# Kernel optimization log

Measured on AMD Instinct MI355X. Metric: run time of the kernel, lower is better.

Reference implementation:

```python
import jax, jax.numpy as jnp
import numpy as np

N = 65536      # total nodes (cells) in batch
E = 262144     # edges per edge type
T = 3          # edge types: row, col, diag
D = 128        # hidden_dim
HG = 4         # gat_heads
DHG = D // HG  # 32, GAT head dim
HH = 4         # hgt_heads
DHH = D // HH  # 32, HGT head dim
B = 32         # boards per batch
SLOPE = 0.2
EPS = 1e-6


def setup_inputs():
    ks = jax.random.split(jax.random.key(0), 32)
    def nrm(i, shape, s=0.05):
        return (jax.random.normal(ks[i], shape) * s).astype(jnp.float32)
    inp = {
        'x_cell': nrm(0, (N, D), 1.0),
        'z_h': nrm(1, (B, D), 1.0),
        'x_cell_embedded': nrm(2, (N, D), 1.0),
        'edge_index': jax.random.randint(ks[3], (T, 2, E), 0, N, dtype=jnp.int32),
        'batch_size': B,
        # GAT conv 1 (one GATConv per edge type, summed)
        'gat1_W': nrm(4, (T, D, D), 0.09),
        'gat1_asrc': nrm(5, (T, HG, DHG), 0.12),
        'gat1_adst': nrm(6, (T, HG, DHG), 0.12),
        'gat1_b': jnp.zeros((T, D), jnp.float32),
        # GAT conv 2
        'gat2_W': nrm(7, (T, D, D), 0.09),
        'gat2_asrc': nrm(8, (T, HG, DHG), 0.12),
        'gat2_adst': nrm(9, (T, HG, DHG), 0.12),
        'gat2_b': jnp.zeros((T, D), jnp.float32),
        # RMSNorms
        'norm1_s': jnp.ones((D,), jnp.float32),
        'norm2_s': jnp.ones((D,), jnp.float32),
        'norm3_s': jnp.ones((D,), jnp.float32),
        # HGT (single node type 'cell', T edge types)
        'hgt_Wk': nrm(10, (D, D), 0.09), 'hgt_bk': jnp.zeros((D,), jnp.float32),
        'hgt_Wq': nrm(11, (D, D), 0.09), 'hgt_bq': jnp.zeros((D,), jnp.float32),
        'hgt_Wv': nrm(12, (D, D), 0.09), 'hgt_bv': jnp.zeros((D,), jnp.float32),
        'hgt_arel': nrm(13, (T, HH, DHH, DHH), 0.15),
        'hgt_mrel': nrm(14, (T, HH, DHH, DHH), 0.15),
        'hgt_prel': jnp.ones((T, HH), jnp.float32),
        'hgt_Wo': nrm(15, (D, D), 0.09), 'hgt_bo': jnp.zeros((D,), jnp.float32),
        'hgt_skip': jnp.ones((), jnp.float32),
        # input injection
        'inj_W': nrm(16, (D, D), 0.09), 'inj_b': jnp.zeros((D,), jnp.float32),
        # FiLM
        'film_W1': nrm(17, (D, 2 * D), 0.09), 'film_b1': jnp.zeros((2 * D,), jnp.float32),
        'film_W2': nrm(18, (2 * D, 2 * D), 0.001), 'film_b2': jnp.zeros((2 * D,), jnp.float32),
    }
    return inp


def _rmsnorm(x, scale):
    return scale * x * jax.lax.rsqrt(jnp.mean(x * x, axis=-1, keepdims=True) + EPS)


def _res(x_old, x_new, scale):
    return jax.nn.leaky_relu(x_old + _rmsnorm(x_new, scale), SLOPE)


def _gat_sum(x, W, asrc, adst, b, src, dst):
    """HeteroConv(sum) over T GATConvs (concat heads, add_self_loops)."""
    loop = jnp.arange(N, dtype=src.dtype)
    def one(Wt, a_s, a_d, bt, s, t):
        s = jnp.concatenate([s, loop])   # self loops
        t = jnp.concatenate([t, loop])
        h = (x @ Wt).reshape(N, HG, DHG)             # [N,H,Dh]
        alpha_src = (h * a_s).sum(-1)                # [N,H]
        alpha_dst = (h * a_d).sum(-1)
        e = jax.nn.leaky_relu(alpha_src[s] + alpha_dst[t], SLOPE)  # [E+N,H]
        m = jax.ops.segment_max(e, t, num_segments=N)
        ex = jnp.exp(e - m[t])
        denom = jax.ops.segment_sum(ex, t, num_segments=N)
        alpha = ex / (denom[t] + 1e-16)
        out = jax.ops.segment_sum(alpha[:, :, None] * h[s], t, num_segments=N)
        return out.reshape(N, D) + bt
    return jax.vmap(one)(W, asrc, adst, b, src, dst).sum(0)


def _hgt(x, Wk, bk, Wq, bq, Wv, bv, a_rel, m_rel, p_rel, Wo, bo, skip, src, dst):
    k = (x @ Wk + bk).reshape(N, HH, DHH)
    q = (x @ Wq + bq).reshape(N, HH, DHH)
    v = (x @ Wv + bv).reshape(N, HH, DHH)
    # per-edge-type relation transforms at node level, then gather per edge
    k_t = jnp.einsum('nhd,thdf->tnhf', k, a_rel)    # [T,N,H,Dk]
    v_t = jnp.einsum('nhd,thdf->tnhf', v, m_rel)
    k_e = jax.vmap(lambda a, i: a[i])(k_t, src)     # [T,E,H,Dk]
    v_e = jax.vmap(lambda a, i: a[i])(v_t, src)
    score = (q[dst] * k_e).sum(-1) * p_rel[:, None, :] / np.sqrt(DHH)  # [T,E,H]
    score = score.reshape(T * E, HH)
    dst_f = dst.reshape(-1)
    m = jax.ops.segment_max(score, dst_f, num_segments=N)
    ex = jnp.exp(score - m[dst_f])
    denom = jax.ops.segment_sum(ex, dst_f, num_segments=N)
    alpha = ex / (denom[dst_f] + 1e-16)
    agg = jax.ops.segment_sum(alpha[:, :, None] * v_e.reshape(T * E, HH, DHH),
                              dst_f, num_segments=N)          # [N,H,Dk]
    out = jax.nn.gelu(agg.reshape(N, D), approximate=False) @ Wo + bo
    sig = jax.nn.sigmoid(skip)
    return sig * out + (1.0 - sig) * x


def _film(nodes, z_h, W1, b1, W2, b2, bsz):
    gb = jax.nn.gelu(z_h @ W1 + b1, approximate=False) @ W2 + b2  # [B,2D]
    gamma, beta = jnp.split(gb, 2, axis=-1)
    gamma = 0.1 * jnp.tanh(gamma)
    beta = 0.1 * jnp.tanh(beta)
    c = N // bsz
    out = (1.0 + gamma)[:, None, :] * nodes.reshape(bsz, c, D) + beta[:, None, :]
    return out.reshape(N, D)


def reference(x_cell, z_h, x_cell_embedded,
              gat1_W, gat1_asrc, gat1_adst, gat1_b,
              gat2_W, gat2_asrc, gat2_adst, gat2_b,
              norm1_s, norm2_s, norm3_s,
              hgt_Wk, hgt_bk, hgt_Wq, hgt_bq, hgt_Wv, hgt_bv,
              hgt_arel, hgt_mrel, hgt_prel, hgt_Wo, hgt_bo, hgt_skip,
              inj_W, inj_b, film_W1, film_b1, film_W2, film_b2,
              edge_index, batch_size):
    src = edge_index[:, 0]
    dst = edge_index[:, 1]
    x1 = _res(x_cell, _gat_sum(x_cell, gat1_W, gat1_asrc, gat1_adst, gat1_b, src, dst), norm1_s)
    x2 = _res(x1, _gat_sum(x1, gat2_W, gat2_asrc, gat2_adst, gat2_b, src, dst), norm2_s)
    x3 = _res(x2, _hgt(x2, hgt_Wk, hgt_bk, hgt_Wq, hgt_bq, hgt_Wv, hgt_bv,
                       hgt_arel, hgt_mrel, hgt_prel, hgt_Wo, hgt_bo, hgt_skip,
                       src, dst), norm3_s)
    x3 = x3 + x_cell_embedded @ inj_W + inj_b
    return _film(x3, z_h, film_W1, film_b1, film_W2, film_b2, batch_size)
```

## Files before the change

kernel.cpp:

```cpp
#include <hip/hip_runtime.h>

#define NN 65536
#define EE 262144
#define ND ((size_t)NN * 128)
#define TBW 132
#define WLP 136
#define NTOT (EE + NN)
#define CSRN (3*EE + 3*NN)

typedef unsigned short u16;
typedef unsigned char u8;
typedef short bf8_t __attribute__((ext_vector_type(8)));
typedef float f32x4 __attribute__((ext_vector_type(4)));
typedef float f32x2 __attribute__((ext_vector_type(2)));

__device__ __forceinline__ float lrelu(float x){ return x > 0.f ? x : 0.2f*x; }
__device__ __forceinline__ float gelu_exact(float x){ return 0.5f*x*(1.f+erff(x*0.70710678118654752f)); }
__device__ __forceinline__ float fexp(float x){ return __expf(x); }
__device__ __forceinline__ u16 f2bf(float f){
    union { float f; unsigned u; } v; v.f = f;
    unsigned u = v.u;
    return (u16)((u + 0x7FFFu + ((u >> 16) & 1u)) >> 16);
}
__device__ __forceinline__ float bf2f(u16 b){
    union { unsigned u; float f; } v; v.u = ((unsigned)b) << 16; return v.f;
}
__device__ __forceinline__ float2 bf2x(unsigned p){
    union { unsigned u; float f; } a, b;
    a.u = (p & 0xFFFFu) << 16; b.u = p & 0xFFFF0000u;
    return make_float2(a.f, b.f);
}
__device__ __forceinline__ unsigned cvt2(float a, float b){
    unsigned r; asm("v_cvt_pk_bf16_f32 %0, %1, %2" : "=v"(r) : "v"(a), "v"(b)); return r;
}
__device__ __forceinline__ unsigned enc_fp8x4(float a, float b, float c, float d){
    int r = __builtin_amdgcn_cvt_pk_fp8_f32(a, b, 0, false);
    r = __builtin_amdgcn_cvt_pk_fp8_f32(c, d, r, true);
    return (unsigned)r;
}

__device__ __forceinline__ void load_af32(const float* __restrict__ X, int row, int lk, bf8_t* af){
    #pragma unroll
    for (int kk = 0; kk < 4; ++kk){
        const float* p = X + (size_t)row*128 + kk*32 + lk*8;
        float4 a = *(const float4*)p;
        float4 b = *(const float4*)(p+4);
        union { bf8_t v; unsigned u[4]; } r;
        r.u[0] = cvt2(a.x, a.y); r.u[1] = cvt2(a.z, a.w);
        r.u[2] = cvt2(b.x, b.y); r.u[3] = cvt2(b.z, b.w);
        af[kk] = r.v;
    }
}
__device__ __forceinline__ void load_af16(const u16* __restrict__ X, int row, int lk, bf8_t* af){
    #pragma unroll
    for (int kk = 0; kk < 4; ++kk)
        af[kk] = *(const bf8_t*)(X + (size_t)row*128 + kk*32 + lk*8);
}

__device__ __forceinline__ void stage_w(const u16* __restrict__ src, u16* __restrict__ wl, int tid){
    #pragma unroll
    for (int j = 0; j < 8; ++j){
        int o = (j*256 + tid)*8;
        bf8_t v = *(const bf8_t*)(src + o);
        *(bf8_t*)(wl + ((o>>7)*WLP + (o&127))) = v;
    }
}

__device__ __forceinline__ void mfma_l1_acc(const bf8_t* af, const u16* __restrict__ wl,
                                            int lr, int lk, f32x4* acc){
    #pragma unroll
    for (int kk = 0; kk < 4; ++kk){
        bf8_t B[8];
        #pragma unroll
        for (int nt = 0; nt < 8; ++nt)
            B[nt] = *(const bf8_t*)&wl[(nt*16+lr)*WLP + kk*32 + lk*8];
        #pragma unroll
        for (int nt = 0; nt < 8; ++nt)
            acc[nt] = __builtin_amdgcn_mfma_f32_16x16x32_bf16(af[kk], B[nt], acc[nt], 0, 0, 0);
    }
}
__device__ __forceinline__ void mfma_l1(const bf8_t* af, const u16* __restrict__ wl,
                                        int lr, int lk, f32x4* acc){
    #pragma unroll
    for (int i = 0; i < 8; ++i) acc[i] = (f32x4){0.f,0.f,0.f,0.f};
    mfma_l1_acc(af, wl, lr, lk, acc);
}
__device__ __forceinline__ void mfma_l2(const bf8_t* af0, const bf8_t* af1,
                                        const u16* __restrict__ wl,
                                        int lr, int lk, f32x4* acc0, f32x4* acc1){
    #pragma unroll
    for (int i = 0; i < 8; ++i){ acc0[i] = (f32x4){0.f,0.f,0.f,0.f}; acc1[i] = (f32x4){0.f,0.f,0.f,0.f}; }
    #pragma unroll
    for (int kk = 0; kk < 4; ++kk){
        bf8_t B[8];
        #pragma unroll
        for (int nt = 0; nt < 8; ++nt)
            B[nt] = *(const bf8_t*)&wl[(nt*16+lr)*WLP + kk*32 + lk*8];
        #pragma unroll
        for (int nt = 0; nt < 8; ++nt){
            acc0[nt] = __builtin_amdgcn_mfma_f32_16x16x32_bf16(af0[kk], B[nt], acc0[nt], 0, 0, 0);
            acc1[nt] = __builtin_amdgcn_mfma_f32_16x16x32_bf16(af1[kk], B[nt], acc1[nt], 0, 0, 0);
        }
    }
}
__device__ __forceinline__ void mfma_bd1_acc(const bf8_t* af, const u16* __restrict__ Bp,
                                             int lr, int lk, f32x4* acc){
    bf8_t B[8];
    #pragma unroll
    for (int nt = 0; nt < 8; ++nt)
        B[nt] = *(const bf8_t*)&Bp[nt*512 + lr*32 + lk*8];
    #pragma unroll
    for (int nt = 0; nt < 8; ++nt)
        acc[nt] = __builtin_amdgcn_mfma_f32_16x16x32_bf16(af[nt>>1], B[nt], acc[nt], 0, 0, 0);
}
__device__ __forceinline__ void mfma_bd2(const bf8_t* af0, const bf8_t* af1,
                                         const u16* __restrict__ Bp,
                                         int lr, int lk, f32x4* acc0, f32x4* acc1){
    bf8_t B[8];
    #pragma unroll
    for (int nt = 0; nt < 8; ++nt)
        B[nt] = *(const bf8_t*)&Bp[nt*512 + lr*32 + lk*8];
    #pragma unroll
    for (int nt = 0; nt < 8; ++nt){
        acc0[nt] = __builtin_amdgcn_mfma_f32_16x16x32_bf16(af0[nt>>1], B[nt], (f32x4){0.f,0.f,0.f,0.f}, 0, 0, 0);
        acc1[nt] = __builtin_amdgcn_mfma_f32_16x16x32_bf16(af1[nt>>1], B[nt], (f32x4){0.f,0.f,0.f,0.f}, 0, 0, 0);
    }
}

__device__ __forceinline__ void acc_to_tb(u16 (*tbw)[TBW], const f32x4* acc, int lr, int lk, const float* bias){
    asm volatile("s_waitcnt lgkmcnt(0)" ::: "memory");
    #pragma unroll
    for (int nt = 0; nt < 8; ++nt){
        int col = nt*16 + lr;
        float badd = bias ? bias[col] : 0.f;
        #pragma unroll
        for (int i = 0; i < 4; ++i) tbw[lk*4+i][col] = f2bf(acc[nt][i] + badd);
    }
    asm volatile("s_waitcnt lgkmcnt(0)" ::: "memory");
}
__device__ __forceinline__ void acc_to_tb_gelu(u16 (*tbw)[TBW], const f32x4* acc, int lr, int lk){
    asm volatile("s_waitcnt lgkmcnt(0)" ::: "memory");
    #pragma unroll
    for (int nt = 0; nt < 8; ++nt){
        int col = nt*16 + lr;
        #pragma unroll
        for (int i = 0; i < 4; ++i) tbw[lk*4+i][col] = f2bf(gelu_exact(acc[nt][i]));
    }
    asm volatile("s_waitcnt lgkmcnt(0)" ::: "memory");
}
__device__ __forceinline__ void tb_store(const u16 (*tbw)[TBW], u16* __restrict__ O, size_t rowstride, int rowbase, int lr, int lk){
    #pragma unroll
    for (int c = 0; c < 4; ++c){
        bf8_t v = *(const bf8_t*)&tbw[c*4+lk][lr*8];
        *(bf8_t*)(O + (size_t)(rowbase + c*4 + lk)*rowstride + lr*8) = v;
    }
}
__device__ __forceinline__ void tb_store_fp8(const u16 (*tbw)[TBW], u8* __restrict__ O, size_t rowstride, int rowbase, int lr, int lk){
    #pragma unroll
    for (int c = 0; c < 4; ++c){
        bf8_t v = *(const bf8_t*)&tbw[c*4+lk][lr*8];
        float f[8];
        #pragma unroll
        for (int j = 0; j < 8; ++j) f[j] = bf2f((u16)v[j]);
        uint2 o2;
        o2.x = enc_fp8x4(f[0], f[1], f[2], f[3]);
        o2.y = enc_fp8x4(f[4], f[5], f[6], f[7]);
        *(uint2*)(O + (size_t)(rowbase + c*4 + lk)*rowstride + lr*8) = o2;
    }
}
__device__ __forceinline__ void tb_frags(const u16 (*tbw)[TBW], int lr, int lk, bf8_t* ha){
    #pragma unroll
    for (int kk = 0; kk < 4; ++kk) ha[kk] = *(const bf8_t*)&tbw[lr][kk*32 + lk*8];
}
__device__ __forceinline__ void tb_rows(const u16 (*tbw)[TBW], int lr, int lk, bf8_t* rw){
    #pragma unroll
    for (int c = 0; c < 4; ++c) rw[c] = *(const bf8_t*)&tbw[c*4+lk][lr*8];
}

__global__ __launch_bounds__(256) void xcast_k(const float* __restrict__ X, u16* __restrict__ O){
    size_t gid = (size_t)blockIdx.x*256 + threadIdx.x;
    const float* p = X + gid*8;
    float4 a = *(const float4*)p;
    float4 b = *(const float4*)(p+4);
    union { bf8_t v; unsigned u[4]; } r;
    r.u[0] = cvt2(a.x, a.y); r.u[1] = cvt2(a.z, a.w);
    r.u[2] = cvt2(b.x, b.y); r.u[3] = cvt2(b.z, b.w);
    *(bf8_t*)(O + gid*8) = r.v;
}

__global__ __launch_bounds__(256) void wpack_k(
    const float* __restrict__ g1W, const float* __restrict__ g2W,
    const float* __restrict__ Wk, const float* __restrict__ Wq, const float* __restrict__ Wv,
    const float* __restrict__ Wo, const float* __restrict__ injW,
    const float* __restrict__ arel, const float* __restrict__ mrel,
    const float* __restrict__ g1as, const float* __restrict__ g1ad,
    const float* __restrict__ g2as, const float* __restrict__ g2ad,
    u16* __restrict__ wp, u16* __restrict__ wpa)
{
    int b = blockIdx.x, tid = threadIdx.x;
    if (b < 11) {
        const float* src;
        if (b < 3) src = g1W + b*16384;
        else if (b < 6) src = g2W + (b-3)*16384;
        else if (b == 6) src = Wk;
        else if (b == 7) src = Wq;
        else if (b == 8) src = Wv;
        else if (b == 9) src = Wo;
        else src = injW;
        u16* dst = wp + (size_t)b*16384;
        for (int idx = tid; idx < 16384; idx += 256) {
            int n = idx >> 7, k = idx & 127;
            dst[idx] = f2bf(src[k*128 + n]);
        }
    } else if (b < 17) {
        int rel2 = (b < 14);
        const float* src = rel2 ? (arel + (b-11)*4096) : (mrel + (b-14)*4096);
        u16* dst = wp + (size_t)11*16384 + (size_t)(b-11)*4096;
        for (int idx = tid; idx < 4096; idx += 256) {
            int nt = idx >> 9, rest = idx & 511;
            int lr = rest >> 5, kp = rest & 31;
            int h = nt >> 1, c = (nt & 1)*16 + lr;
            float v = rel2 ? src[h*1024 + c*32 + kp] : src[h*1024 + kp*32 + c];
            dst[idx] = f2bf(v);
        }
    } else {
        for (int idx = tid; idx < 6*2048; idx += 256) {
            int m = idx >> 11;
            int j = idx & 2047;
            int cg = j >> 7, k = j & 127;
            const float* as = (m < 3) ? g1as : g2as;
            const float* ad = (m < 3) ? g1ad : g2ad;
            int t = (m < 3) ? m : m - 3;
            float v = 0.f;
            if (cg < 4)      { if ((k>>5)==cg)   v = as[t*128 + cg*32 + (k&31)]; }
            else if (cg < 8) { int g = cg-4; if ((k>>5)==g) v = ad[t*128 + g*32 + (k&31)]; }
            wpa[idx] = f2bf(v);
        }
    }
}

__global__ __launch_bounds__(256, 3) void gat_gemm3_k(const u16* __restrict__ Xb,
    const u16* __restrict__ wpg, const u16* __restrict__ wpa,
    u16* __restrict__ hb, float* __restrict__ alsb, float* __restrict__ aldb)
{
    __shared__ __align__(16) u16 wl[128*WLP];
    __shared__ __align__(16) u16 tb[4][16][TBW];
    const int tid = threadIdx.x, wave = tid>>6, lane = tid&63, lr = lane&15, lk = lane>>4;
    const int t = blockIdx.y;
    const int rw0 = blockIdx.x*128 + wave*32;
    bf8_t af0[4], af1[4];
    load_af16(Xb, rw0 + lr, lk, af0);
    load_af16(Xb, rw0 + 16 + lr, lk, af1);
    stage_w(wpg + t*16384, wl, tid);
    bf8_t Ba[4];
    #pragma unroll
    for (int kk = 0; kk < 4; ++kk)
        Ba[kk] = *(const bf8_t*)&wpa[t*2048 + lr*128 + kk*32 + lk*8];
    __syncthreads();
    f32x4 acc0[8], acc1[8];
    mfma_l2(af0, af1, wl, lr, lk, acc0, acc1);
    u16* h = hb + (size_t)t*ND;
    float* alst = alsb + (size_t)t*NN*4;
    float* aldt = aldb + (size_t)t*NN*4;
    {
        acc_to_tb(tb[wave], acc0, lr, lk, nullptr);
        tb_store(tb[wave], h, 128, rw0, lr, lk);
        bf8_t ha[4]; tb_frags(tb[wave], lr, lk, ha);
        f32x4 a2 = (f32x4){0.f,0.f,0.f,0.f};
        #pragma unroll
        for (int kk = 0; kk < 4; ++kk)
            a2 = __builtin_amdgcn_mfma_f32_16x16x32_bf16(ha[kk], Ba[kk], a2, 0, 0, 0);
        if (lr < 8){
            float* dp = (lr < 4) ? alst : aldt;
            int g = lr & 3;
            #pragma unroll
            for (int i = 0; i < 4; ++i) dp[(size_t)(rw0 + lk*4 + i)*4 + g] = a2[i];
        }
    }
    {
        acc_to_tb(tb[wave], acc1, lr, lk, nullptr);
        tb_store(tb[wave], h, 128, rw0 + 16, lr, lk);
        bf8_t ha[4]; tb_frags(tb[wave], lr, lk, ha);
        f32x4 a2 = (f32x4){0.f,0.f,0.f,0.f};
        #pragma unroll
        for (int kk = 0; kk < 4; ++kk)
            a2 = __builtin_amdgcn_mfma_f32_16x16x32_bf16(ha[kk], Ba[kk], a2, 0, 0, 0);
        if (lr < 8){
            float* dp = (lr < 4) ? alst : aldt;
            int g = lr & 3;
            #pragma unroll
            for (int i = 0; i < 4; ++i) dp[(size_t)(rw0 + 16 + lk*4 + i)*4 + g] = a2[i];
        }
    }
}

__global__ __launch_bounds__(256, 3) void hgt_proj_k(const u16* __restrict__ X,
    const u16* __restrict__ wpk, const u16* __restrict__ wpq, const u16* __restrict__ wpv,
    const u16* __restrict__ wpad,
    const float* __restrict__ bk, const float* __restrict__ bq, const float* __restrict__ bv,
    u8* __restrict__ kvb, u16* __restrict__ qtb)
{
    __shared__ __align__(16) u16 wl[128*WLP];
    __shared__ __align__(16) u16 tb[4][16][TBW];
    const int tid = threadIdx.x, wave = tid>>6, lane = tid&63, lr = lane&15, lk = lane>>4;
    const int task = blockIdx.y;
    const int rw0 = blockIdx.x*128 + wave*32;
    bf8_t af0[4], af1[4];
    load_af16(X, rw0 + lr, lk, af0);
    load_af16(X, rw0 + 16 + lr, lk, af1);
    f32x4 acc0[8], acc1[8];
    if (task == 0) {
        stage_w(wpk, wl, tid);
        __syncthreads();
        mfma_l2(af0, af1, wl, lr, lk, acc0, acc1);
        acc_to_tb(tb[wave], acc0, lr, lk, bk); tb_store_fp8(tb[wave], kvb, 256, rw0, lr, lk);
        acc_to_tb(tb[wave], acc1, lr, lk, bk); tb_store_fp8(tb[wave], kvb, 256, rw0 + 16, lr, lk);
    } else if (task == 1) {
        stage_w(wpv, wl, tid);
        __syncthreads();
        mfma_l2(af0, af1, wl, lr, lk, acc0, acc1);
        acc_to_tb(tb[wave], acc0, lr, lk, bv); tb_store_fp8(tb[wave], kvb + 128, 256, rw0, lr, lk);
        acc_to_tb(tb[wave], acc1, lr, lk, bv); tb_store_fp8(tb[wave], kvb + 128, 256, rw0 + 16, lr, lk);
    } else {
        const int t = task - 2;
        stage_w(wpq, wl, tid);
        __syncthreads();
        mfma_l2(af0, af1, wl, lr, lk, acc0, acc1);
        bf8_t ha0[4], ha1[4];
        acc_to_tb(tb[wave], acc0, lr, lk, bq); tb_frags(tb[wave], lr, lk, ha0);
        acc_to_tb(tb[wave], acc1, lr, lk, bq); tb_frags(tb[wave], lr, lk, ha1);
        mfma_bd2(ha0, ha1, wpad + t*4096, lr, lk, acc0, acc1);
        u16* o = qtb + (size_t)t*ND;
        acc_to_tb(tb[wave], acc0, lr, lk, nullptr); tb_store(tb[wave], o, 128, rw0, lr, lk);
        acc_to_tb(tb[wave], acc1, lr, lk, nullptr); tb_store(tb[wave], o, 128, rw0 + 16, lr, lk);
    }
}

__global__ __launch_bounds__(256) void hist_k(const int* __restrict__ ei, int* __restrict__ cnt){
    int gid = blockIdx.x*256 + threadIdx.x;
    int t = gid / EE, e = gid - t*EE;
    int d = ei[t*2*EE + EE + e];
    atomicAdd(&cnt[t*NN + d], 1);
}
__global__ __launch_bounds__(256) void scanA_k(const int* __restrict__ cnt, int* __restrict__ s0off, int* __restrict__ parts){
    __shared__ int sums[256];
    int b = blockIdx.x; int base = b * 1024;
    int tid = threadIdx.x;
    int v[4]; int tsum = 0;
    #pragma unroll
    for (int i = 0; i < 4; ++i){
        int n = base + tid*4 + i;
        v[i] = cnt[n] + cnt[NN+n] + cnt[2*NN+n] + 3;
        tsum += v[i];
    }
    sums[tid] = tsum; __syncthreads();
    for (int ofs = 1; ofs < 256; ofs <<= 1) {
        int a = (tid >= ofs) ? sums[tid-ofs] : 0;
        __syncthreads();
        sums[tid] += a;
        __syncthreads();
    }
    int run = sums[tid] - tsum;
    #pragma unroll
    for (int i = 0; i < 4; ++i){ s0off[base + tid*4 + i] = run; run += v[i]; }
    if (tid == 255) parts[b] = sums[255];
}
__global__ void scan2_k(int* parts){
    if (threadIdx.x == 0 && blockIdx.x == 0) {
        int run = 0;
        for (int i = 0; i < 64; ++i) { int v = parts[i]; parts[i] = run; run += v; }
    }
}
__global__ __launch_bounds__(256) void scanB_k(const int* __restrict__ cnt, int* __restrict__ s0off,
                                               int* __restrict__ s1off, int* __restrict__ s2off,
                                               const int* __restrict__ parts){
    int b = blockIdx.x; int base = b * 1024;
    int add = parts[b];
    #pragma unroll
    for (int i = 0; i < 4; ++i){
        int n = base + threadIdx.x*4 + i;
        int m = s0off[n] + add;
        int c0 = cnt[n], c1 = cnt[NN+n];
        s0off[n] = m;
        s1off[n] = m + c0 + 1;
        s2off[n] = m + c0 + c1 + 2;
    }
    if (b == 0 && threadIdx.x == 0) s0off[NN] = CSRN;
}
__global__ __launch_bounds__(256) void selffill_k(const int* __restrict__ s0off, const int* __restrict__ s1off,
                                                  const int* __restrict__ s2off, int* __restrict__ csrc){
    int gid = blockIdx.x*256 + threadIdx.x;
    int t = gid / NN, n = gid - t*NN;
    int pos = (t==0) ? s0off[n] : (t==1 ? s1off[n] : s2off[n]);
    csrc[pos] = n;
}
__global__ __launch_bounds__(256) void scatter_k(const int* __restrict__ ei,
    const int* __restrict__ s0off, const int* __restrict__ s1off, const int* __restrict__ s2off,
    int* __restrict__ cur, int* __restrict__ csrc, int* __restrict__ posmap){
    int gid = blockIdx.x*256 + threadIdx.x;
    int t = gid / EE, e = gid - t*EE;
    int s = ei[t*2*EE + e];
    int d = ei[t*2*EE + EE + e];
    int p = atomicAdd(&cur[t*NN + d], 1);
    int basep = (t==0) ? s0off[d] : (t==1 ? s1off[d] : s2off[d]);
    int pos = basep + 1 + p;
    csrc[pos] = s;
    posmap[t*EE + e] = pos;
}

__global__ __launch_bounds__(256) void alpha_k(const float* __restrict__ alsb, const float* __restrict__ aldb,
    const int* __restrict__ ei, const int* __restrict__ posmap,
    const int* __restrict__ s0off, const int* __restrict__ s1off, const int* __restrict__ s2off,
    float4* __restrict__ ab)
{
    int gid = blockIdx.x*256 + threadIdx.x;
    int t = gid / NTOT, r = gid - t*NTOT;
    int s, d, pos;
    if (r < EE) {
        s = ei[t*2*EE + r];
        d = ei[t*2*EE + EE + r];
        pos = posmap[t*EE + r];
    } else {
        int n = r - EE;
        s = n; d = n;
        pos = (t==0) ? s0off[n] : (t==1 ? s1off[n] : s2off[n]);
    }
    const float* As = alsb + ((size_t)t*NN + s)*4;
    const float* Ad = aldb + ((size_t)t*NN + d)*4;
    float4 o;
    o.x = fexp(lrelu(As[0] + Ad[0]));
    o.y = fexp(lrelu(As[1] + Ad[1]));
    o.z = fexp(lrelu(As[2] + Ad[2]));
    o.w = fexp(lrelu(As[3] + Ad[3]));
    ab[pos] = o;
}

__global__ __launch_bounds__(256) void gat_aggres_k(const u16* __restrict__ hb,
    const float* __restrict__ abf,
    const int* __restrict__ s0off, const int* __restrict__ s1off, const int* __restrict__ s2off,
    const int* __restrict__ csrc,
    const float* __restrict__ bias3, const u16* __restrict__ xoldb,
    const float* __restrict__ scale, u16* __restrict__ outb)
{
    int gid = blockIdx.x*256 + threadIdx.x;
    int node = gid >> 6, lane = gid & 63;
    int eh = lane >> 5, hh = (lane >> 3) & 3, cp = lane & 7;
    int ch = hh*32 + cp*4;
    int segb[4] = { s0off[node], s1off[node], s2off[node], s0off[node+1] };
    float a[4] = {0.f, 0.f, 0.f, 0.f};
    #pragma unroll
    for (int t = 0; t < 3; ++t) {
        const u16* h = hb + (size_t)t*ND;
        int beg = segb[t], end = segb[t+1];
        float ds = 0.f, s0 = 0.f, s1 = 0.f, s2 = 0.f, s3 = 0.f;
        for (int pos = beg; pos < end; pos += 4) {
            int p0 = pos + eh, p1 = pos + 2 + eh;
            int v0 = (p0 < end), v1 = (p1 < end);
            int q0 = v0 ? p0 : beg, q1 = v1 ? p1 : beg;
            int sA = csrc[q0], sB = csrc[q1];
            float alA = abf[(size_t)q0*4 + hh];
            float alB = abf[(size_t)q1*4 + hh];
            uint2 hA = *(const uint2*)&h[(size_t)sA*128 + ch];
            uint2 hB = *(const uint2*)&h[(size_t)sB*128 + ch];
            alA = v0 ? alA : 0.f;
            alB = v1 ? alB : 0.f;
            float2 wA0 = bf2x(hA.x), wA1 = bf2x(hA.y);
            float2 wB0 = bf2x(hB.x), wB1 = bf2x(hB.y);
            ds += alA + alB;
            s0 += alA*wA0.x + alB*wB0.x;
            s1 += alA*wA0.y + alB*wB0.y;
            s2 += alA*wA1.x + alB*wB1.x;
            s3 += alA*wA1.y + alB*wB1.y;
        }
        ds += __shfl_xor(ds, 32);
        s0 += __shfl_xor(s0, 32);
        s1 += __shfl_xor(s1, 32);
        s2 += __shfl_xor(s2, 32);
        s3 += __shfl_xor(s3, 32);
        float inv = 1.f/(ds + 1e-16f);
        a[0] += s0*inv; a[1] += s1*inv; a[2] += s2*inv; a[3] += s3*inv;
    }
    float4 b0 = *(const float4*)&bias3[ch];
    float4 b1 = *(const float4*)&bias3[128 + ch];
    float4 b2 = *(const float4*)&bias3[256 + ch];
    a[0] += b0.x + b1.x + b2.x;
    a[1] += b0.y + b1.y + b2.y;
    a[2] += b0.z + b1.z + b2.z;
    a[3] += b0.w + b1.w + b2.w;
    float ssum = a[0]*a[0] + a[1]*a[1] + a[2]*a[2] + a[3]*a[3];
    ssum += __shfl_xor(ssum, 1); ssum += __shfl_xor(ssum, 2);
    ssum += __shfl_xor(ssum, 4); ssum += __shfl_xor(ssum, 8);
    ssum += __shfl_xor(ssum, 16);
    float r = rsqrtf(ssum*(1.f/128.f) + 1e-6f);
    float4 sc = *(const float4*)&scale[ch];
    size_t off = (size_t)node*128 + ch;
    uint2 xo = *(const uint2*)&xoldb[off];
    float2 p0 = bf2x(xo.x), p1 = bf2x(xo.y);
    float y0 = lrelu(p0.x + sc.x*a[0]*r);
    float y1 = lrelu(p0.y + sc.y*a[1]*r);
    float y2 = lrelu(p1.x + sc.z*a[2]*r);
    float y3 = lrelu(p1.y + sc.w*a[3]*r);
    uint2 o2; o2.x = cvt2(y0, y1); o2.y = cvt2(y2, y3);
    *(uint2*)&outb[off] = o2;
}

__global__ __launch_bounds__(256) void hgt_agg_k(const u8* __restrict__ kvb,
    const u16* __restrict__ qtb, const float* __restrict__ prel,
    const int* __restrict__ s0off, const int* __restrict__ s1off, const int* __restrict__ s2off,
    const int* __restrict__ csrc, u16* __restrict__ pb)
{
    int gid = blockIdx.x*256 + threadIdx.x;
    int node = gid >> 6, lane = gid & 63;
    int eh = lane >> 5, hh = (lane >> 3) & 3, cp = lane & 7;
    int ch = hh*32 + cp*4;
    const float S = 0.17677669529663689f;
    int segb[4] = { s0off[node], s1off[node], s2off[node], s0off[node+1] };
    float dsum = 0.f;
    float ac[3][4];
    #pragma unroll
    for (int t = 0; t < 3; ++t){ ac[t][0]=0.f; ac[t][1]=0.f; ac[t][2]=0.f; ac[t][3]=0.f; }
    #pragma unroll
    for (int t = 0; t < 3; ++t) {
        float ph = prel[t*4 + hh] * S;
        uint2 qw = *(const uint2*)&qtb[(size_t)t*ND + (size_t)node*128 + ch];
        float2 q0 = bf2x(qw.x), q1 = bf2x(qw.y);
        int self = segb[t];
        int beg = self + 1, end = segb[t+1];
        for (int pos = beg; pos < end; pos += 4) {
            int p0 = pos + eh, p1 = pos + 2 + eh;
            int v0 = (p0 < end), v1 = (p1 < end);
            int qp0 = v0 ? p0 : self, qp1 = v1 ? p1 : self;
            int sA = csrc[qp0], sB = csrc[qp1];
            size_t rA = (size_t)sA*256 + ch, rB = (size_t)sB*256 + ch;
            unsigned kA = *(const unsigned*)&kvb[rA], kB = *(const unsigned*)&kvb[rB];
            unsigned vA = *(const unsigned*)&kvb[rA + 128], vB = *(const unsigned*)&kvb[rB + 128];
            f32x2 kA0 = __builtin_amdgcn_cvt_pk_f32_fp8((int)kA, false);
            f32x2 kA1 = __builtin_amdgcn_cvt_pk_f32_fp8((int)kA, true);
            f32x2 kB0 = __builtin_amdgcn_cvt_pk_f32_fp8((int)kB, false);
            f32x2 kB1 = __builtin_amdgcn_cvt_pk_f32_fp8((int)kB, true);
            float scA = kA0[0]*q0.x + kA0[1]*q0.y + kA1[0]*q1.x + kA1[1]*q1.y;
            float scB = kB0[0]*q0.x + kB0[1]*q0.y + kB1[0]*q1.x + kB1[1]*q1.y;
            scA += __shfl_xor(scA, 1); scB += __shfl_xor(scB, 1);
            scA += __shfl_xor(scA, 2); scB += __shfl_xor(scB, 2);
            scA += __shfl_xor(scA, 4); scB += __shfl_xor(scB, 4);
            float eA = v0 ? fexp(scA*ph) : 0.f;
            float eB = v1 ? fexp(scB*ph) : 0.f;
            f32x2 vA0 = __builtin_amdgcn_cvt_pk_f32_fp8((int)vA, false);
            f32x2 vA1 = __builtin_amdgcn_cvt_pk_f32_fp8((int)vA, true);
            f32x2 vB0 = __builtin_amdgcn_cvt_pk_f32_fp8((int)vB, false);
            f32x2 vB1 = __builtin_amdgcn_cvt_pk_f32_fp8((int)vB, true);
            dsum += eA + eB;
            ac[t][0] += eA*vA0[0] + eB*vB0[0];
            ac[t][1] += eA*vA0[1] + eB*vB0[1];
            ac[t][2] += eA*vA1[0] + eB*vB1[0];
            ac[t][3] += eA*vA1[1] + eB*vB1[1];
        }
    }
    dsum += __shfl_xor(dsum, 32);
    #pragma unroll
    for (int t = 0; t < 3; ++t){
        ac[t][0] += __shfl_xor(ac[t][0], 32);
        ac[t][1] += __shfl_xor(ac[t][1], 32);
        ac[t][2] += __shfl_xor(ac[t][2], 32);
        ac[t][3] += __shfl_xor(ac[t][3], 32);
    }
    float inv = 1.f/(dsum + 1e-16f);
    size_t o = (size_t)node*128 + ch;
    #pragma unroll
    for (int t = 0; t < 3; ++t){
        uint2 o2;
        o2.x = cvt2(ac[t][0]*inv, ac[t][1]*inv);
        o2.y = cvt2(ac[t][2]*inv, ac[t][3]*inv);
        *(uint2*)&pb[(size_t)t*ND + o] = o2;
    }
}

__global__ __launch_bounds__(256, 3) void final_k(const u16* __restrict__ pb,
    const u16* __restrict__ wpmd, const u16* __restrict__ wpo, const float* __restrict__ bo,
    const u16* __restrict__ x2b, const float* __restrict__ skipp, const float* __restrict__ scale,
    const float* __restrict__ xemb, const u16* __restrict__ wpinj, const float* __restrict__ injb,
    const float* __restrict__ gbuf, const int* __restrict__ bszp,
    float* __restrict__ out)
{
    __shared__ __align__(16) u16 wl[128*WLP];
    __shared__ __align__(16) u16 tb[4][16][TBW];
    const int tid = threadIdx.x, wave = tid>>6, lane = tid&63, lr = lane&15, lk = lane>>4;
    const int rw = blockIdx.x*64 + wave*16;
    stage_w(wpo, wl, tid);
    bf8_t e0[4];
    load_af32(xemb, rw + lr, lk, e0);
    f32x4 acc[8];
    #pragma unroll
    for (int i = 0; i < 8; ++i) acc[i] = (f32x4){0.f,0.f,0.f,0.f};
    #pragma unroll
    for (int t = 0; t < 3; ++t){
        bf8_t a0[4]; load_af16(pb + (size_t)t*ND, rw + lr, lk, a0);
        mfma_bd1_acc(a0, wpmd + t*4096, lr, lk, acc);
    }
    bf8_t ga[4];
    acc_to_tb_gelu(tb[wave], acc, lr, lk);
    tb_frags(tb[wave], lr, lk, ga);
    __syncthreads();
    mfma_l1(ga, wl, lr, lk, acc);
    bf8_t hw[4];
    acc_to_tb(tb[wave], acc, lr, lk, bo);
    tb_rows(tb[wave], lr, lk, hw);
    __syncthreads();
    stage_w(wpinj, wl, tid);
    __syncthreads();
    mfma_l1(e0, wl, lr, lk, acc);
    bf8_t in[4];
    acc_to_tb(tb[wave], acc, lr, lk, injb);
    tb_rows(tb[wave], lr, lk, in);
    const float sig = 1.f/(1.f + expf(-skipp[0]));
    const int cpb = NN / *bszp;
    float4 sca = *(const float4*)&scale[lr*8];
    float4 scb = *(const float4*)&scale[lr*8 + 4];
    #pragma unroll
    for (int c = 0; c < 4; ++c){
        int row = rw + c*4 + lk;
        bf8_t x8 = *(const bf8_t*)(x2b + (size_t)row*128 + lr*8);
        float x[8], v[8];
        float ssl = 0.f;
        #pragma unroll
        for (int j = 0; j < 8; ++j){
            x[j] = bf2f((u16)x8[j]);
            float h = bf2f((u16)hw[c][j]);
            v[j] = sig*h + (1.f - sig)*x[j];
            ssl += v[j]*v[j];
        }
        ssl += __shfl_xor(ssl, 1); ssl += __shfl_xor(ssl, 2);
        ssl += __shfl_xor(ssl, 4); ssl += __shfl_xor(ssl, 8);
        float rq = rsqrtf(ssl*(1.f/128.f) + 1e-6f);
        const float* gr = gbuf + (row / cpb)*256;
        float4 g0 = *(const float4*)&gr[lr*8];
        float4 g1 = *(const float4*)&gr[lr*8 + 4];
        float4 b0 = *(const float4*)&gr[128 + lr*8];
        float4 b1 = *(const float4*)&gr[128 + lr*8 + 4];
        float4 oA, oB;
        #pragma unroll
        for (int j = 0; j < 8; ++j){
            float scj = (j < 4) ? ((const float*)&sca)[j] : ((const float*)&scb)[j-4];
            float y = lrelu(x[j] + scj*v[j]*rq);
            float hf = y + bf2f((u16)in[c][j]);
            float gj = (j < 4) ? ((const float*)&g0)[j] : ((const float*)&g1)[j-4];
            float bj = (j < 4) ? ((const float*)&b0)[j] : ((const float*)&b1)[j-4];
            float ov = (1.f + gj)*hf + bj;
            if (j < 4) ((float*)&oA)[j] = ov; else ((float*)&oB)[j-4] = ov;
        }
        *(float4*)(out + (size_t)row*128 + lr*8)     = oA;
        *(float4*)(out + (size_t)row*128 + lr*8 + 4) = oB;
    }
}

__global__ __launch_bounds__(256) void film_k(const float* __restrict__ z,
    const float* __restrict__ W1, const float* __restrict__ b1,
    const float* __restrict__ W2, const float* __restrict__ b2,
    float* __restrict__ gb)
{
    __shared__ float zr[128];
    __shared__ float g1[256];
    int r = blockIdx.x, tid = threadIdx.x;
    if (tid < 128) zr[tid] = z[r*128 + tid];
    __syncthreads();
    float s = b1[tid];
    for (int k = 0; k < 128; ++k) s += zr[k]*W1[k*256 + tid];
    g1[tid] = gelu_exact(s);
    __syncthreads();
    float s2 = b2[tid];
    for (int k = 0; k < 256; ++k) s2 += g1[k]*W2[k*256 + tid];
    gb[r*256 + tid] = 0.1f*tanhf(s2);
}

extern "C" void kernel_launch(void* const* d_in, const int* in_sizes, int n_in,
                              void* d_out, int out_size, void* d_ws, size_t ws_size,
                              hipStream_t stream)
{
    const float* x_cell = (const float*)d_in[0];
    const float* z_h    = (const float*)d_in[1];
    const float* x_emb  = (const float*)d_in[2];
    const int*   eidx   = (const int*)d_in[3];
    const int*   bszp   = (const int*)d_in[4];
    const float* g1W  = (const float*)d_in[5];
    const float* g1as = (const float*)d_in[6];
    const float* g1ad = (const float*)d_in[7];
    const float* g1b  = (const float*)d_in[8];
    const float* g2W  = (const float*)d_in[9];
    const float* g2as = (const float*)d_in[10];
    const float* g2ad = (const float*)d_in[11];
    const float* g2b  = (const float*)d_in[12];
    const float* n1s  = (const float*)d_in[13];
    const float* n2s  = (const float*)d_in[14];
    const float* n3s  = (const float*)d_in[15];
    const float* Wk   = (const float*)d_in[16];
    const float* bk   = (const float*)d_in[17];
    const float* Wq   = (const float*)d_in[18];
    const float* bq   = (const float*)d_in[19];
    const float* Wv   = (const float*)d_in[20];
    const float* bv   = (const float*)d_in[21];
    const float* arel = (const float*)d_in[22];
    const float* mrel = (const float*)d_in[23];
    const float* prel = (const float*)d_in[24];
    const float* Wo   = (const float*)d_in[25];
    const float* bo   = (const float*)d_in[26];
    const float* skipp= (const float*)d_in[27];
    const float* injW = (const float*)d_in[28];
    const float* injb = (const float*)d_in[29];
    const float* fW1  = (const float*)d_in[30];
    const float* fb1  = (const float*)d_in[31];
    const float* fW2  = (const float*)d_in[32];
    const float* fb2  = (const float*)d_in[33];

    u16* wp   = (u16*)d_ws;
    u16* wpa  = wp + (size_t)17*16384;
    float4* ab = (float4*)(wpa + 6*2048);
    u16* x0b  = (u16*)(ab + CSRN);
    u16* x1b  = x0b + ND;
    u16* x2b  = x1b + ND;
    u8*  kvb  = (u8*)(x2b + ND);
    u16* pb   = (u16*)(kvb + (size_t)NN*256);
    u16* hb   = pb + 3*ND;
    float* alsb = (float*)(hb + 3*ND);
    float* aldb = alsb + (size_t)3*NN*4;
    float* gbuf = aldb + (size_t)3*NN*4;
    int* s0off  = (int*)(gbuf + 32*256);
    int* s1off  = s0off + (NN+1);
    int* s2off  = s1off + NN;
    int* csrc   = s2off + NN;
    int* posmap = csrc + CSRN;
    int* tmpc   = posmap + 3*EE;
    int* cur    = tmpc + 3*NN;
    int* parts  = cur + 3*NN;

    u16* qtb = hb;
    float* outp = (float*)d_out;

    const u16* wpg1 = wp;
    const u16* wpg2 = wp + (size_t)3*16384;
    const u16* wpk  = wp + (size_t)6*16384;
    const u16* wpq  = wp + (size_t)7*16384;
    const u16* wpv  = wp + (size_t)8*16384;
    const u16* wpo  = wp + (size_t)9*16384;
    const u16* wpinj= wp + (size_t)10*16384;
    const u16* wpad = wp + (size_t)11*16384;
    const u16* wpmd = wpad + (size_t)3*4096;

    wpack_k<<<18, 256, 0, stream>>>(g1W, g2W, Wk, Wq, Wv, Wo, injW, arel, mrel,
                                    g1as, g1ad, g2as, g2ad, wp, wpa);
    xcast_k<<<(int)(ND/2048), 256, 0, stream>>>(x_cell, x0b);

    hipMemsetAsync(tmpc, 0, 3*NN*sizeof(int), stream);
    hist_k<<<3*EE/256, 256, 0, stream>>>(eidx, tmpc);
    scanA_k<<<64, 256, 0, stream>>>(tmpc, s0off, parts);
    scan2_k<<<1, 64, 0, stream>>>(parts);
    scanB_k<<<64, 256, 0, stream>>>(tmpc, s0off, s1off, s2off, parts);
    selffill_k<<<3*NN/256, 256, 0, stream>>>(s0off, s1off, s2off, csrc);
    hipMemsetAsync(cur, 0, 3*NN*sizeof(int), stream);
    scatter_k<<<3*EE/256, 256, 0, stream>>>(eidx, s0off, s1off, s2off, cur, csrc, posmap);

    int B = in_sizes[1] / 128;
    film_k<<<B, 256, 0, stream>>>(z_h, fW1, fb1, fW2, fb2, gbuf);

    gat_gemm3_k<<<dim3(512,3), 256, 0, stream>>>(x0b, wpg1, wpa, hb, alsb, aldb);
    alpha_k<<<3*NTOT/256, 256, 0, stream>>>(alsb, aldb, eidx, posmap, s0off, s1off, s2off, ab);
    gat_aggres_k<<<16384, 256, 0, stream>>>(hb, (const float*)ab, s0off, s1off, s2off, csrc,
                                            g1b, x0b, n1s, x1b);

    gat_gemm3_k<<<dim3(512,3), 256, 0, stream>>>(x1b, wpg2, wpa + 3*2048, hb, alsb, aldb);
    alpha_k<<<3*NTOT/256, 256, 0, stream>>>(alsb, aldb, eidx, posmap, s0off, s1off, s2off, ab);
    gat_aggres_k<<<16384, 256, 0, stream>>>(hb, (const float*)ab, s0off, s1off, s2off, csrc,
                                            g2b, x1b, n2s, x2b);

    hgt_proj_k<<<dim3(512,5), 256, 0, stream>>>(x2b, wpk, wpq, wpv, wpad,
                                                bk, bq, bv, kvb, qtb);
    hgt_agg_k<<<16384, 256, 0, stream>>>(kvb, qtb, prel, s0off, s1off, s2off, csrc, pb);

    final_k<<<1024, 256, 0, stream>>>(pb, wpmd, wpo, bo, x2b, skipp, n3s,
                                      x_emb, wpinj, injb, gbuf, bszp, outp);
}
```

Before: 540.9 us.

## Move input-injection GEMM into HGT projection kernel and interleave per-type aggregation output

The x_cell_embedded @ inj_W projection moves out of final_k into an extra task row of hgt_proj_k. It is written as a bf16 buffer that final_k reads in its epilogue, which removes a weight restage and two barriers from final_k. The hgt_agg output layout also changes from three separate N×128 planes to one interleaved N×384 row per node, so final_k's three per-type loads come from a single contiguous row. The cost is an extra bf16 N×128 write and read through global memory, plus one more grid row in the projection kernel.

After: 544.2 us. Within noise of the previous version (+0.6%).

```diff
diff --git a/kernel.cpp b/kernel.cpp
--- a/kernel.cpp
+++ b/kernel.cpp
@@ -66,8 +66,10 @@
     }
 }
 
-__device__ __forceinline__ void mfma_l1_acc(const bf8_t* af, const u16* __restrict__ wl,
-                                            int lr, int lk, f32x4* acc){
+__device__ __forceinline__ void mfma_l1(const bf8_t* af, const u16* __restrict__ wl,
+                                        int lr, int lk, f32x4* acc){
+    #pragma unroll
+    for (int i = 0; i < 8; ++i) acc[i] = (f32x4){0.f,0.f,0.f,0.f};
     #pragma unroll
     for (int kk = 0; kk < 4; ++kk){
         bf8_t B[8];
@@ -78,12 +80,6 @@
         for (int nt = 0; nt < 8; ++nt)
             acc[nt] = __builtin_amdgcn_mfma_f32_16x16x32_bf16(af[kk], B[nt], acc[nt], 0, 0, 0);
     }
-}
-__device__ __forceinline__ void mfma_l1(const bf8_t* af, const u16* __restrict__ wl,
-                                        int lr, int lk, f32x4* acc){
-    #pragma unroll
-    for (int i = 0; i < 8; ++i) acc[i] = (f32x4){0.f,0.f,0.f,0.f};
-    mfma_l1_acc(af, wl, lr, lk, acc);
 }
 __device__ __forceinline__ void mfma_l2(const bf8_t* af0, const bf8_t* af1,
                                         const u16* __restrict__ wl,
@@ -296,19 +292,31 @@
 
 __global__ __launch_bounds__(256, 3) void hgt_proj_k(const u16* __restrict__ X,
     const u16* __restrict__ wpk, const u16* __restrict__ wpq, const u16* __restrict__ wpv,
-    const u16* __restrict__ wpad,
+    const u16* __restrict__ wpad, const u16* __restrict__ wpinj, const float* __restrict__ xembf,
     const float* __restrict__ bk, const float* __restrict__ bq, const float* __restrict__ bv,
-    u8* __restrict__ kvb, u16* __restrict__ qtb)
+    const float* __restrict__ injb,
+    u8* __restrict__ kvb, u16* __restrict__ qtb, u16* __restrict__ injv)
 {
     __shared__ __align__(16) u16 wl[128*WLP];
     __shared__ __align__(16) u16 tb[4][16][TBW];
     const int tid = threadIdx.x, wave = tid>>6, lane = tid&63, lr = lane&15, lk = lane>>4;
     const int task = blockIdx.y;
     const int rw0 = blockIdx.x*128 + wave*32;
+    f32x4 acc0[8], acc1[8];
+    if (task == 2) {
+        bf8_t e0[4], e1[4];
+        load_af32(xembf, rw0 + lr, lk, e0);
+        load_af32(xembf, rw0 + 16 + lr, lk, e1);
+        stage_w(wpinj, wl, tid);
+        __syncthreads();
+        mfma_l2(e0, e1, wl, lr, lk, acc0, acc1);
+        acc_to_tb(tb[wave], acc0, lr, lk, injb); tb_store(tb[wave], injv, 128, rw0, lr, lk);
+        acc_to_tb(tb[wave], acc1, lr, lk, injb); tb_store(tb[wave], injv, 128, rw0 + 16, lr, lk);
+        return;
+    }
     bf8_t af0[4], af1[4];
     load_af16(X, rw0 + lr, lk, af0);
     load_af16(X, rw0 + 16 + lr, lk, af1);
-    f32x4 acc0[8], acc1[8];
     if (task == 0) {
         stage_w(wpk, wl, tid);
         __syncthreads();
@@ -322,7 +330,7 @@
         acc_to_tb(tb[wave], acc0, lr, lk, bv); tb_store_fp8(tb[wave], kvb + 128, 256, rw0, lr, lk);
         acc_to_tb(tb[wave], acc1, lr, lk, bv); tb_store_fp8(tb[wave], kvb + 128, 256, rw0 + 16, lr, lk);
     } else {
-        const int t = task - 2;
+        const int t = task - 3;
         stage_w(wpq, wl, tid);
         __syncthreads();
         mfma_l2(af0, af1, wl, lr, lk, acc0, acc1);
@@ -565,20 +573,20 @@
         ac[t][3] += __shfl_xor(ac[t][3], 32);
     }
     float inv = 1.f/(dsum + 1e-16f);
-    size_t o = (size_t)node*128 + ch;
+    size_t o = (size_t)node*384 + ch;
     #pragma unroll
     for (int t = 0; t < 3; ++t){
         uint2 o2;
         o2.x = cvt2(ac[t][0]*inv, ac[t][1]*inv);
         o2.y = cvt2(ac[t][2]*inv, ac[t][3]*inv);
-        *(uint2*)&pb[(size_t)t*ND + o] = o2;
+        *(uint2*)&pb[o + (size_t)t*128] = o2;
     }
 }
 
 __global__ __launch_bounds__(256, 3) void final_k(const u16* __restrict__ pb,
     const u16* __restrict__ wpmd, const u16* __restrict__ wpo, const float* __restrict__ bo,
     const u16* __restrict__ x2b, const float* __restrict__ skipp, const float* __restrict__ scale,
-    const float* __restrict__ xemb, const u16* __restrict__ wpinj, const float* __restrict__ injb,
+    const u16* __restrict__ injv,
     const float* __restrict__ gbuf, const int* __restrict__ bszp,
     float* __restrict__ out)
 {
@@ -587,15 +595,19 @@
     const int tid = threadIdx.x, wave = tid>>6, lane = tid&63, lr = lane&15, lk = lane>>4;
     const int rw = blockIdx.x*64 + wave*16;
     stage_w(wpo, wl, tid);
-    bf8_t e0[4];
-    load_af32(xemb, rw + lr, lk, e0);
     f32x4 acc[8];
     #pragma unroll
     for (int i = 0; i < 8; ++i) acc[i] = (f32x4){0.f,0.f,0.f,0.f};
-    #pragma unroll
-    for (int t = 0; t < 3; ++t){
-        bf8_t a0[4]; load_af16(pb + (size_t)t*ND, rw + lr, lk, a0);
-        mfma_bd1_acc(a0, wpmd + t*4096, lr, lk, acc);
+    {
+        const u16* pr = pb + (size_t)(rw + lr)*384;
+        #pragma unroll
+        for (int t = 0; t < 3; ++t){
+            bf8_t a0[4];
+            #pragma unroll
+            for (int kk = 0; kk < 4; ++kk)
+                a0[kk] = *(const bf8_t*)(pr + t*128 + kk*32 + lk*8);
+            mfma_bd1_acc(a0, wpmd + t*4096, lr, lk, acc);
+        }
     }
     bf8_t ga[4];
     acc_to_tb_gelu(tb[wave], acc, lr, lk);
@@ -605,13 +617,6 @@
     bf8_t hw[4];
     acc_to_tb(tb[wave], acc, lr, lk, bo);
     tb_rows(tb[wave], lr, lk, hw);
-    __syncthreads();
-    stage_w(wpinj, wl, tid);
-    __syncthreads();
-    mfma_l1(e0, wl, lr, lk, acc);
-    bf8_t in[4];
-    acc_to_tb(tb[wave], acc, lr, lk, injb);
-    tb_rows(tb[wave], lr, lk, in);
     const float sig = 1.f/(1.f + expf(-skipp[0]));
     const int cpb = NN / *bszp;
     float4 sca = *(const float4*)&scale[lr*8];
@@ -620,6 +625,7 @@
     for (int c = 0; c < 4; ++c){
         int row = rw + c*4 + lk;
         bf8_t x8 = *(const bf8_t*)(x2b + (size_t)row*128 + lr*8);
+        bf8_t i8 = *(const bf8_t*)(injv + (size_t)row*128 + lr*8);
         float x[8], v[8];
         float ssl = 0.f;
         #pragma unroll
@@ -642,7 +648,7 @@
         for (int j = 0; j < 8; ++j){
             float scj = (j < 4) ? ((const float*)&sca)[j] : ((const float*)&scb)[j-4];
             float y = lrelu(x[j] + scj*v[j]*rq);
-            float hf = y + bf2f((u16)in[c][j]);
+            float hf = y + bf2f((u16)i8[j]);
             float gj = (j < 4) ? ((const float*)&g0)[j] : ((const float*)&g1)[j-4];
             float bj = (j < 4) ? ((const float*)&b0)[j] : ((const float*)&b1)[j-4];
             float ov = (1.f + gj)*hf + bj;
@@ -720,7 +726,8 @@
     u8*  kvb  = (u8*)(x2b + ND);
     u16* pb   = (u16*)(kvb + (size_t)NN*256);
     u16* hb   = pb + 3*ND;
-    float* alsb = (float*)(hb + 3*ND);
+    u16* injv = hb + 3*ND;
+    float* alsb = (float*)(injv + ND);
     float* aldb = alsb + (size_t)3*NN*4;
     float* gbuf = aldb + (size_t)3*NN*4;
     int* s0off  = (int*)(gbuf + 32*256);
@@ -771,10 +778,10 @@
     gat_aggres_k<<<16384, 256, 0, stream>>>(hb, (const float*)ab, s0off, s1off, s2off, csrc,
                                             g2b, x1b, n2s, x2b);
 
-    hgt_proj_k<<<dim3(512,5), 256, 0, stream>>>(x2b, wpk, wpq, wpv, wpad,
-                                                bk, bq, bv, kvb, qtb);
+    hgt_proj_k<<<dim3(512,6), 256, 0, stream>>>(x2b, wpk, wpq, wpv, wpad, wpinj, x_emb,
+                                                bk, bq, bv, injb, kvb, qtb, injv);
     hgt_agg_k<<<16384, 256, 0, stream>>>(kvb, qtb, prel, s0off, s1off, s2off, csrc, pb);
 
     final_k<<<1024, 256, 0, stream>>>(pb, wpmd, wpo, bo, x2b, skipp, n3s,
-                                      x_emb, wpinj, injb, gbuf, bszp, outp);
-}
+                                      injv, gbuf, bszp, outp);
+}
```
